# Optimization experiments

Measured on AMD Instinct MI355X. Metric: run time of the kernel, lower is better.

The kernel has to match this reference:

```python
import jax, jax.numpy as jnp
import numpy as np

B, S0 = 16, 511
D = 512    # encoder_output_dim
HG = 256   # graph_rnn_hidden_graph
HE = 256   # graph_rnn_hidden_edge (must equal HG: h_prev[0] = graph_state)
T = 128    # tag_representation_dim
M = 32     # graph_rnn_m
S = S0 + 1 # after head-sentinel prepend


def setup_inputs() -> dict:
    ks = iter(jax.random.split(jax.random.key(0), 40))
    def U(shape, fan):
        # torch RNN/Linear default init: U(-1/sqrt(fan), 1/sqrt(fan))
        return jax.random.uniform(next(ks), shape, jnp.float32, -1.0, 1.0) / np.sqrt(fan)
    return {
        'input': jax.random.normal(next(ks), (B, S0, D), jnp.float32),
        'sentinel': jax.random.normal(next(ks), (D,), jnp.float32),
        'g_Wih0': U((HG, D), HG), 'g_Whh0': U((HG, HG), HG), 'g_bih0': U((HG,), HG), 'g_bhh0': U((HG,), HG),
        'g_Wih1': U((HG, HG), HG), 'g_Whh1': U((HG, HG), HG), 'g_bih1': U((HG,), HG), 'g_bhh1': U((HG,), HG),
        'e_Wih0': U((HE, 1), HE), 'e_Whh0': U((HE, HE), HE), 'e_bih0': U((HE,), HE), 'e_bhh0': U((HE,), HE),
        'e_Wih1': U((HE, HE), HE), 'e_Whh1': U((HE, HE), HE), 'e_bih1': U((HE,), HE), 'e_bhh1': U((HE,), HE),
        'cls_W': U((1, HE), HE), 'cls_b': U((1,), HE),
        'head_W': U((T, HG), HG), 'head_b': U((T,), HG),
        'dep_W': U((T, HG), HG), 'dep_b': U((T,), HG),
        'mask': jnp.ones((B, S0), jnp.int32),
        'head_indices': jax.random.randint(next(ks), (B, S0), 0, S0, jnp.int32),
    }


def _rnn_layer(x, W_ih, W_hh, b_ih, b_hh):
    # Elman RNN layer (tanh), batch_first, h0 = 0. x: [B, S, Din] -> [B, S, H]
    xw = jnp.einsum('bsd,hd->bsh', x, W_ih) + b_ih + b_hh  # hoist input GEMM out of scan
    h0 = jnp.zeros((x.shape[0], W_hh.shape[0]), x.dtype)
    def step(h, xw_t):
        h = jnp.tanh(xw_t + h @ W_hh.T)
        return h, h
    _, ys = jax.lax.scan(step, h0, jnp.swapaxes(xw, 0, 1))
    return jnp.swapaxes(ys, 0, 1)


def _forward(input, sentinel, g_Wih0, g_Whh0, g_bih0, g_bhh0, g_Wih1, g_Whh1, g_bih1, g_bhh1,
             e_Wih0, e_Whh0, e_bih0, e_bhh0, e_Wih1, e_Whh1, e_bih1, e_bhh1,
             cls_W, cls_b, head_W, head_b, dep_W, dep_b, mask, head_indices):
    Bv = input.shape[0]
    # prepend head sentinel / prepend_ones
    x = jnp.concatenate([jnp.broadcast_to(sentinel, (Bv, 1, D)), input], axis=1)   # [B,S,D]
    mask_f = jnp.concatenate([jnp.ones((Bv, 1), mask.dtype), mask], axis=1)        # [B,S]
    # graph_pass: 2-layer tanh RNN; pad_packed_sequence zeroes padded timesteps
    h = _rnn_layer(x, g_Wih0, g_Whh0, g_bih0, g_bhh0)
    gs = _rnn_layer(h, g_Wih1, g_Whh1, g_bih1, g_bhh1)                             # [B,S,HG]
    gs = gs * mask_f[..., None].astype(gs.dtype)
    N = Bv * S
    gt = gs.reshape(N, HG)
    def estep(carry, _):
        xe, h0, h1 = carry
        h0 = jnp.tanh(xe @ e_Wih0.T + e_bih0 + e_bhh0 + h0 @ e_Whh0.T)
        h1 = jnp.tanh(h0 @ e_Wih1.T + e_bih1 + e_bhh1 + h1 @ e_Whh1.T)
        p = jax.nn.sigmoid(h1 @ cls_W.T + cls_b)   # [N,1]
        return (p, h0, h1), p[:, 0]
    init = (jnp.ones((N, 1), gs.dtype), gt, jnp.zeros((N, HE), gs.dtype))
    _, probs = jax.lax.scan(estep, init, None, length=M)                           # [M,N]
    A = jnp.concatenate([jnp.ones((1, N), gs.dtype), probs], axis=0).T.reshape(Bv, S, M + 1)
    # reshape_adj: scatter the M-band back into a [B,S,S] matrix, then transpose
    Ab = A[:, :, 1:]                                                               # [B,S,M]
    i = jnp.arange(S)[:, None]
    j = jnp.arange(S)[None, :]
    start = jnp.maximum(0, i - M)
    valid = (j >= start) & (j < i)
    midx = jnp.clip(j - start, 0, M - 1)                                           # [S,S]
    gathered = Ab[:, jnp.arange(S)[:, None], midx]                                 # [B,S,S]
    arc_logits = jnp.swapaxes(jnp.where(valid[None], gathered, jnp.zeros((), gs.dtype)), 1, 2)
    # tag heads (dropout = identity at inference)
    head_tag = jax.nn.elu(jnp.einsum('bsh,th->bst', gs, head_W) + head_b)
    dep_tag = jax.nn.elu(jnp.einsum('bsh,th->bst', gs, dep_W) + dep_b)
    return head_tag, dep_tag, arc_logits


def reference(input, sentinel, g_Wih0, g_Whh0, g_bih0, g_bhh0, g_Wih1, g_Whh1, g_bih1, g_bhh1,
              e_Wih0, e_Whh0, e_bih0, e_bhh0, e_Wih1, e_Whh1, e_bih1, e_bhh1,
              cls_W, cls_b, head_W, head_b, dep_W, dep_b, mask, head_indices):
    return _forward(input, sentinel, g_Wih0, g_Whh0, g_bih0, g_bhh0, g_Wih1, g_Whh1, g_bih1, g_bhh1,
                    e_Wih0, e_Whh0, e_bih0, e_bhh0, e_Wih1, e_Whh1, e_bih1, e_bhh1,
                    cls_W, cls_b, head_W, head_b, dep_W, dep_b, mask, head_indices)
```

## Files before the change

kernel.cpp:

```cpp
#include <hip/hip_runtime.h>

typedef unsigned short u16;
typedef short s8v __attribute__((ext_vector_type(8)));
typedef float f4v __attribute__((ext_vector_type(4)));

__device__ __forceinline__ float bf2f(u16 s) {
  unsigned u = ((unsigned)s) << 16;
  return __builtin_bit_cast(float, u);
}
__device__ __forceinline__ u16 f2bf(float f) {
  unsigned u = __builtin_bit_cast(unsigned, f);
  unsigned r = u + 0x7fffu + ((u >> 16) & 1u);
  return (u16)(r >> 16);
}
__device__ __forceinline__ s8v load8bf(const u16* p) {
  return __builtin_bit_cast(s8v, *(const uint4*)p);
}
__device__ __forceinline__ f4v mfma16(s8v a, s8v b, f4v c) {
  return __builtin_amdgcn_mfma_f32_16x16x32_bf16(a, b, c, 0, 0, 0);
}
__device__ __forceinline__ s8v pin8(s8v x) {
  union { s8v v; unsigned u[4]; } t;
  t.v = x;
  asm volatile("" : "+v"(t.u[0]), "+v"(t.u[1]), "+v"(t.u[2]), "+v"(t.u[3]));
  return t.v;
}
__device__ __forceinline__ void barrier_lds() {
  asm volatile("s_waitcnt lgkmcnt(0)\n\ts_barrier" ::: "memory");
}
__device__ __forceinline__ void cvt8(const float* p, s8v& hi, s8v& lo) {
  float4 x0 = ((const float4*)p)[0];
  float4 x1 = ((const float4*)p)[1];
  float v[8] = {x0.x, x0.y, x0.z, x0.w, x1.x, x1.y, x1.z, x1.w};
  union { s8v v; u16 a[8]; } H, L;
#pragma unroll
  for (int i = 0; i < 8; ++i) {
    u16 h = f2bf(v[i]);
    H.a[i] = h;
    L.a[i] = f2bf(v[i] - bf2f(h));
  }
  hi = H.v;
  lo = L.v;
}
__device__ __forceinline__ float fast_tanh(float x) {
  float t = __builtin_amdgcn_exp2f(x * 2.885390081777927f);
  return 1.f - 2.f * __builtin_amdgcn_rcpf(t + 1.f);
}
__device__ __forceinline__ float fast_sigmoid(float x) {
  float t = __builtin_amdgcn_exp2f(x * -1.4426950408889634f);
  return __builtin_amdgcn_rcpf(1.f + t);
}

__global__ void k_prep(const float* __restrict__ W0, const float* __restrict__ W1,
                       u16* __restrict__ whh0b, u16* __restrict__ whh1b,
                       const float* __restrict__ E0, const float* __restrict__ E1,
                       const float* __restrict__ E2, u16* __restrict__ B0,
                       u16* __restrict__ B1, u16* __restrict__ B2,
                       const float* __restrict__ gW0, u16* __restrict__ gw0hi,
                       u16* __restrict__ gw0lo, const float* __restrict__ gW1,
                       u16* __restrict__ gw1hi, u16* __restrict__ gw1lo,
                       const float* __restrict__ hW, u16* __restrict__ hWhi,
                       u16* __restrict__ hWlo, const float* __restrict__ dW,
                       u16* __restrict__ dWhi, u16* __restrict__ dWlo,
                       const int* __restrict__ mask, float* __restrict__ maskfb) {
  int t = blockIdx.x * 256 + threadIdx.x;
  if (t < 131072) {
    int layer = t >> 16;
    int idx = t & 65535;
    const float* W = layer ? W1 : W0;
    u16* dst = layer ? whh1b : whh0b;
    dst[idx] = f2bf(W[idx]);
  } else if (t < 327680) {
    int c = t - 131072;
    int which = c >> 16;
    int idx = c & 65535;
    const float* src = which == 0 ? E0 : (which == 1 ? E1 : E2);
    u16* dst = which == 0 ? B0 : (which == 1 ? B1 : B2);
    dst[idx] = f2bf(src[idx]);
  } else if (t < 589824) {
    const float* src;
    u16 *dhi, *dlo;
    int idx;
    if (t < 458752) { idx = t - 327680; src = gW0; dhi = gw0hi; dlo = gw0lo; }
    else if (t < 524288) { idx = t - 458752; src = gW1; dhi = gw1hi; dlo = gw1lo; }
    else if (t < 557056) { idx = t - 524288; src = hW; dhi = hWhi; dlo = hWlo; }
    else { idx = t - 557056; src = dW; dhi = dWhi; dlo = dWlo; }
    float v = src[idx];
    u16 h = f2bf(v);
    dhi[idx] = h;
    dlo[idx] = f2bf(v - bf2f(h));
  } else if (t < 598016) {
    int c = t - 589824;
    int s = c >> 4, b = c & 15;
    maskfb[c] = (s == 0) ? 1.f : (float)mask[b * 511 + s - 1];
  }
}

__launch_bounds__(256)
__global__ void k_xw0(const float* __restrict__ input, const float* __restrict__ sentinel,
                      const u16* __restrict__ Whi, const u16* __restrict__ Wlo,
                      const float* __restrict__ b1, const float* __restrict__ b2,
                      float* __restrict__ outxw) {
  const int l = threadIdx.x & 63;
  const int wv = threadIdx.x >> 6;
  const int l15 = l & 15, q = l >> 4;
  const int row0 = blockIdx.x * 64 + wv * 16;
  const int col0 = blockIdx.y * 64;
  int row = row0 + l15;
  int s = row & 511, b = row >> 9;
  const float* aptr = (s == 0) ? sentinel : input + (((size_t)(b * 511 + s - 1)) << 9);
  f4v acc[4];
#pragma unroll
  for (int i = 0; i < 4; ++i) acc[i] = (f4v){0.f, 0.f, 0.f, 0.f};
#pragma unroll
  for (int kt = 0; kt < 16; ++kt) {
    int k0 = kt * 32 + q * 8;
    s8v ah, al;
    cvt8(aptr + k0, ah, al);
#pragma unroll
    for (int nt = 0; nt < 4; ++nt) {
      int j = col0 + nt * 16 + l15;
      s8v wh = load8bf(Whi + ((size_t)j << 9) + k0);
      s8v wl = load8bf(Wlo + ((size_t)j << 9) + k0);
      acc[nt] = mfma16(ah, wh, acc[nt]);
      acc[nt] = mfma16(al, wh, acc[nt]);
      acc[nt] = mfma16(ah, wl, acc[nt]);
    }
  }
#pragma unroll
  for (int nt = 0; nt < 4; ++nt) {
    int col = col0 + nt * 16 + l15;
    float bias = b1[col] + b2[col];
#pragma unroll
    for (int r = 0; r < 4; ++r) {
      int rr = row0 + q * 4 + r;
      outxw[((size_t)rr << 8) + col] = acc[nt][r] + bias;
    }
  }
}

__launch_bounds__(256)
__global__ void k_gemm(const float* __restrict__ A, const u16* __restrict__ Whi,
                       const u16* __restrict__ Wlo, const float* __restrict__ b1,
                       const float* __restrict__ b2, float* __restrict__ outf,
                       int K, int J, int act) {
  const int l = threadIdx.x & 63;
  const int wv = threadIdx.x >> 6;
  const int l15 = l & 15, q = l >> 4;
  const int row0 = blockIdx.x * 64 + wv * 16;
  const int col0 = blockIdx.y * 64;
  const float* aptr = A + (size_t)(row0 + l15) * K;
  f4v acc[4];
#pragma unroll
  for (int i = 0; i < 4; ++i) acc[i] = (f4v){0.f, 0.f, 0.f, 0.f};
  const int nkt = K >> 5;
  for (int kt = 0; kt < nkt; ++kt) {
    int k0 = kt * 32 + q * 8;
    s8v ah, al;
    cvt8(aptr + k0, ah, al);
#pragma unroll
    for (int nt = 0; nt < 4; ++nt) {
      int j = col0 + nt * 16 + l15;
      s8v wh = load8bf(Whi + (size_t)j * K + k0);
      s8v wl = load8bf(Wlo + (size_t)j * K + k0);
      acc[nt] = mfma16(ah, wh, acc[nt]);
      acc[nt] = mfma16(al, wh, acc[nt]);
      acc[nt] = mfma16(ah, wl, acc[nt]);
    }
  }
#pragma unroll
  for (int nt = 0; nt < 4; ++nt) {
    int col = col0 + nt * 16 + l15;
    float bias = b1[col] + (b2 ? b2[col] : 0.f);
#pragma unroll
    for (int r = 0; r < 4; ++r) {
      int rr = row0 + q * 4 + r;
      float v = acc[nt][r] + bias;
      if (act) v = v > 0.f ? v : (__builtin_amdgcn_exp2f(v * 1.4426950408889634f) - 1.f);
      outf[(size_t)rr * J + col] = v;
    }
  }
}

__launch_bounds__(512, 2)
__global__ void k_scan_f(const float* __restrict__ xw, const u16* __restrict__ W0b,
                         const u16* __restrict__ Wxb, const u16* __restrict__ W1b,
                         const float* __restrict__ bih1, const float* __restrict__ bhh1,
                         float* __restrict__ outf, const float* __restrict__ maskf) {
  __shared__ u16 H1[2][272];
  __shared__ u16 H2[2][272];
  __shared__ float XW2[2][272];
  __shared__ float mtab[512];
  const int tid = threadIdx.x;
  const int l = tid & 63, wv = tid >> 6;
  const int l15 = l & 15, q = l >> 4;
  const int b = blockIdx.x;

  s8v w0[2][8], wx[2][8], w1[2][8];
#pragma unroll
  for (int nt = 0; nt < 2; ++nt) {
    int j = wv * 32 + nt * 16 + l15;
#pragma unroll
    for (int kt = 0; kt < 8; ++kt) {
      int off = (j << 8) + kt * 32 + q * 8;
      w0[nt][kt] = pin8(load8bf(W0b + off));
      wx[nt][kt] = pin8(load8bf(Wxb + off));
      w1[nt][kt] = pin8(load8bf(W1b + off));
    }
  }
  if (tid < 256) {
    H1[0][tid] = 0; H1[1][tid] = 0;
    H2[0][tid] = 0; H2[1][tid] = 0;
    XW2[0][tid] = 0.f; XW2[1][tid] = 0.f;
  }
  if (tid < 512) mtab[tid] = maskf[tid * 16 + b];

  const int j0 = wv * 32 + l15;
  float b2v[2];
#pragma unroll
  for (int nt = 0; nt < 2; ++nt) b2v[nt] = bih1[j0 + nt * 16] + bhh1[j0 + nt * 16];
  __syncthreads();

  const size_t nbase = (size_t)b << 9;
  const float* xrow = xw + (nbase << 8);
  const int q0 = (q == 0);

  float xA[2], xB[2];
#pragma unroll
  for (int nt = 0; nt < 2; ++nt) {
    xA[nt] = xrow[j0 + nt * 16];
    xB[nt] = xrow[256 + j0 + nt * 16];
  }

  auto STEP = [&](int g, int par, float* xc) {
    const u16* H1r = &H1[par][0];
    const u16* H2r = &H2[par][0];
    f4v a1[2], ax[2], a2[2];
#pragma unroll
    for (int nt = 0; nt < 2; ++nt) {
      a1[nt] = (f4v){xc[nt], 0.f, 0.f, 0.f};
      ax[nt] = (f4v){b2v[nt], 0.f, 0.f, 0.f};
      a2[nt] = (f4v){XW2[par][j0 + nt * 16], 0.f, 0.f, 0.f};
    }
#pragma unroll
    for (int kt = 0; kt < 8; ++kt) {
      s8v h1b = load8bf(H1r + kt * 32 + q * 8);
#pragma unroll
      for (int nt = 0; nt < 2; ++nt) {
        a1[nt] = mfma16(h1b, w0[nt][kt], a1[nt]);
        ax[nt] = mfma16(h1b, wx[nt][kt], ax[nt]);
      }
    }
#pragma unroll
    for (int kt = 0; kt < 8; ++kt) {
      s8v h2b = load8bf(H2r + kt * 32 + q * 8);
#pragma unroll
      for (int nt = 0; nt < 2; ++nt) a2[nt] = mfma16(h2b, w1[nt][kt], a2[nt]);
    }
    if (g < 512) {
      u16* Hw = &H1[1 - par][0];
#pragma unroll
      for (int nt = 0; nt < 2; ++nt) {
        float h = fast_tanh(a1[nt][0]);
        if (q0) Hw[j0 + nt * 16] = f2bf(h);
      }
    }
    if (g >= 1 && g < 513) {
      float* Xw = &XW2[1 - par][0];
#pragma unroll
      for (int nt = 0; nt < 2; ++nt)
        if (q0) Xw[j0 + nt * 16] = ax[nt][0];
    }
    if (g >= 2) {
      int t = g - 2;
      float mf = mtab[t];
      u16* Hw = &H2[1 - par][0];
      float* orow = outf + ((nbase + t) << 8);
#pragma unroll
      for (int nt = 0; nt < 2; ++nt) {
        float h = fast_tanh(a2[nt][0]);
        if (q0) {
          Hw[j0 + nt * 16] = f2bf(h);
          orow[j0 + nt * 16] = h * mf;
        }
      }
    }
  };

  for (int g = 0; g < 514; g += 2) {
    STEP(g, 0, xA);
    int sp = g + 2; if (sp > 511) sp = 511;
#pragma unroll
    for (int nt = 0; nt < 2; ++nt) xA[nt] = xrow[(sp << 8) + j0 + nt * 16];
    barrier_lds();
    STEP(g + 1, 1, xB);
    int sq = g + 3; if (sq > 511) sq = 511;
#pragma unroll
    for (int nt = 0; nt < 2; ++nt) xB[nt] = xrow[(sq << 8) + j0 + nt * 16];
    barrier_lds();
  }
}

__launch_bounds__(512, 2)
__global__ void k_enc(const float* __restrict__ gs,
                      const u16* __restrict__ W0b, const u16* __restrict__ W1b,
                      const u16* __restrict__ W2b, const float* __restrict__ wih0,
                      const float* __restrict__ bih0, const float* __restrict__ bhh0,
                      const float* __restrict__ bih1, const float* __restrict__ bhh1,
                      const float* __restrict__ clsW, const float* __restrict__ clsb,
                      float* __restrict__ Ab) {
  __shared__ __align__(16) u16 hA0[32 * 264];
  __shared__ __align__(16) u16 hA1[32 * 264];
  __shared__ float xe[32];
  __shared__ float b0v[256], w0v[256], b1v[256], clsv[256];
  __shared__ float clsbs;
  const int tid = threadIdx.x;
  const int n0 = blockIdx.x * 32;

  for (int c = tid; c < 8192; c += 512) {
    int row = c >> 8, col = c & 255;
    hA0[row * 264 + col] = f2bf(gs[(((size_t)(n0 + row)) << 8) + col]);
    hA1[row * 264 + col] = 0;
  }
  if (tid < 256) {
    b0v[tid] = bih0[tid] + bhh0[tid];
    w0v[tid] = wih0[tid];
    b1v[tid] = bih1[tid] + bhh1[tid];
    clsv[tid] = clsW[tid];
  }
  if (tid < 32) xe[tid] = 1.0f;
  if (tid == 0) clsbs = clsb[0];

  const int l = tid & 63, wv = tid >> 6;
  const int l15 = l & 15, q = l >> 4;
  const int colbase = wv * 32;

  s8v w0[2][8], w1[2][8], w2[2][8];
#pragma unroll
  for (int nt = 0; nt < 2; ++nt) {
    int jj = colbase + nt * 16 + l15;
#pragma unroll
    for (int kt = 0; kt < 8; ++kt) {
      int off = (jj << 8) + kt * 32 + q * 8;
      w0[nt][kt] = load8bf(W0b + off);
      w1[nt][kt] = load8bf(W1b + off);
      w2[nt][kt] = load8bf(W2b + off);
    }
  }
  __syncthreads();

  for (int m = 0; m < 32; ++m) {
    f4v acc[2][2];
#pragma unroll
    for (int mt = 0; mt < 2; ++mt)
#pragma unroll
      for (int nt = 0; nt < 2; ++nt) acc[mt][nt] = (f4v){0.f, 0.f, 0.f, 0.f};
#pragma unroll
    for (int kt = 0; kt < 8; ++kt) {
#pragma unroll
      for (int mt = 0; mt < 2; ++mt) {
        s8v a = __builtin_bit_cast(s8v, *(const uint4*)&hA0[(mt * 16 + l15) * 264 + kt * 32 + q * 8]);
        acc[mt][0] = mfma16(a, w0[0][kt], acc[mt][0]);
        acc[mt][1] = mfma16(a, w0[1][kt], acc[mt][1]);
      }
    }
    __syncthreads();
#pragma unroll
    for (int nt = 0; nt < 2; ++nt) {
      int col = colbase + nt * 16 + l15;
      float wc = w0v[col], bc = b0v[col];
#pragma unroll
      for (int mt = 0; mt < 2; ++mt)
#pragma unroll
        for (int r = 0; r < 4; ++r) {
          int row = mt * 16 + q * 4 + r;
          float v = acc[mt][nt][r] + xe[row] * wc + bc;
          hA0[row * 264 + col] = f2bf(fast_tanh(v));
        }
    }
    __syncthreads();
#pragma unroll
    for (int mt = 0; mt < 2; ++mt)
#pragma unroll
      for (int nt = 0; nt < 2; ++nt) acc[mt][nt] = (f4v){0.f, 0.f, 0.f, 0.f};
#pragma unroll
    for (int kt = 0; kt < 8; ++kt) {
#pragma unroll
      for (int mt = 0; mt < 2; ++mt) {
        s8v a0 = __builtin_bit_cast(s8v, *(const uint4*)&hA0[(mt * 16 + l15) * 264 + kt * 32 + q * 8]);
        s8v a1 = __builtin_bit_cast(s8v, *(const uint4*)&hA1[(mt * 16 + l15) * 264 + kt * 32 + q * 8]);
        acc[mt][0] = mfma16(a0, w1[0][kt], acc[mt][0]);
        acc[mt][1] = mfma16(a0, w1[1][kt], acc[mt][1]);
        acc[mt][0] = mfma16(a1, w2[0][kt], acc[mt][0]);
        acc[mt][1] = mfma16(a1, w2[1][kt], acc[mt][1]);
      }
    }
    __syncthreads();
#pragma unroll
    for (int nt = 0; nt < 2; ++nt) {
      int col = colbase + nt * 16 + l15;
      float bc = b1v[col];
#pragma unroll
      for (int mt = 0; mt < 2; ++mt)
#pragma unroll
        for (int r = 0; r < 4; ++r) {
          int row = mt * 16 + q * 4 + r;
          float v = acc[mt][nt][r] + bc;
          hA1[row * 264 + col] = f2bf(fast_tanh(v));
        }
    }
    __syncthreads();
    if (tid < 256) {
      int row = tid >> 3, seg = tid & 7;
      float sum = 0.f;
#pragma unroll
      for (int u = 0; u < 4; ++u) {
        int col = seg * 32 + u * 8;
#pragma unroll
        for (int e = 0; e < 8; ++e) sum += bf2f(hA1[row * 264 + col + e]) * clsv[col + e];
      }
      sum += __shfl_down(sum, 4, 8);
      sum += __shfl_down(sum, 2, 8);
      sum += __shfl_down(sum, 1, 8);
      if (seg == 0) {
        float pp = fast_sigmoid(sum + clsbs);
        xe[row] = pp;
        Ab[(((size_t)(n0 + row)) << 5) + m] = pp;
      }
    }
    __syncthreads();
  }
}

__global__ void k_arc(const float* __restrict__ Ab, float* __restrict__ out2) {
  int t = blockIdx.x * 256 + threadIdx.x;
  int b = t >> 18;
  int rem = t & 262143;
  int j = rem >> 9, i = rem & 511;
  int start = i - 32;
  if (start < 0) start = 0;
  float v = 0.f;
  if (j >= start && j < i) v = Ab[((((size_t)b << 9) + i) << 5) + (j - start)];
  out2[t] = v;
}

extern "C" void kernel_launch(void* const* d_in, const int* in_sizes, int n_in,
                              void* d_out, int out_size, void* d_ws, size_t ws_size,
                              hipStream_t stream) {
  const float* input    = (const float*)d_in[0];
  const float* sentinel = (const float*)d_in[1];
  const float* g_Wih0   = (const float*)d_in[2];
  const float* g_Whh0   = (const float*)d_in[3];
  const float* g_bih0   = (const float*)d_in[4];
  const float* g_bhh0   = (const float*)d_in[5];
  const float* g_Wih1   = (const float*)d_in[6];
  const float* g_Whh1   = (const float*)d_in[7];
  const float* g_bih1   = (const float*)d_in[8];
  const float* g_bhh1   = (const float*)d_in[9];
  const float* e_Wih0   = (const float*)d_in[10];
  const float* e_Whh0   = (const float*)d_in[11];
  const float* e_bih0   = (const float*)d_in[12];
  const float* e_bhh0   = (const float*)d_in[13];
  const float* e_Wih1   = (const float*)d_in[14];
  const float* e_Whh1   = (const float*)d_in[15];
  const float* e_bih1   = (const float*)d_in[16];
  const float* e_bhh1   = (const float*)d_in[17];
  const float* cls_W    = (const float*)d_in[18];
  const float* cls_b    = (const float*)d_in[19];
  const float* head_W   = (const float*)d_in[20];
  const float* head_b   = (const float*)d_in[21];
  const float* dep_W    = (const float*)d_in[22];
  const float* dep_b    = (const float*)d_in[23];
  const int* mask       = (const int*)d_in[24];

  float* out = (float*)d_out;
  char* ws = (char*)d_ws;
  float* xw_buf = (float*)ws;
  float* gsb    = (float*)(ws + (16u << 20));
  float* Ab     = (float*)(ws + (24u << 20));
  size_t o = (25u << 20);
  u16* whh0b   = (u16*)(ws + o); o += 128u << 10;
  u16* whh1b   = (u16*)(ws + o); o += 128u << 10;
  float* maskfb= (float*)(ws + o); o += 32u << 10;
  u16* eb0     = (u16*)(ws + o); o += 128u << 10;
  u16* eb1     = (u16*)(ws + o); o += 128u << 10;
  u16* eb2     = (u16*)(ws + o); o += 128u << 10;
  u16* gw0hi   = (u16*)(ws + o); o += 256u << 10;
  u16* gw0lo   = (u16*)(ws + o); o += 256u << 10;
  u16* gw1hi   = (u16*)(ws + o); o += 128u << 10;
  u16* gw1lo   = (u16*)(ws + o); o += 128u << 10;
  u16* hWhi    = (u16*)(ws + o); o += 64u << 10;
  u16* hWlo    = (u16*)(ws + o); o += 64u << 10;
  u16* dWhi    = (u16*)(ws + o); o += 64u << 10;
  u16* dWlo    = (u16*)(ws + o); o += 64u << 10;

  k_prep<<<2336, 256, 0, stream>>>(g_Whh0, g_Whh1, whh0b, whh1b, e_Whh0, e_Wih1, e_Whh1,
                                   eb0, eb1, eb2, g_Wih0, gw0hi, gw0lo, g_Wih1, gw1hi,
                                   gw1lo, head_W, hWhi, hWlo, dep_W, dWhi, dWlo,
                                   mask, maskfb);
  k_xw0<<<dim3(128, 4), 256, 0, stream>>>(input, sentinel, gw0hi, gw0lo, g_bih0, g_bhh0,
                                          xw_buf);
  k_scan_f<<<16, 512, 0, stream>>>(xw_buf, whh0b, gw1hi, whh1b, g_bih1, g_bhh1,
                                   gsb, maskfb);
  k_gemm<<<dim3(128, 2), 256, 0, stream>>>(gsb, hWhi, hWlo, head_b, nullptr, out,
                                           256, 128, 1);
  k_gemm<<<dim3(128, 2), 256, 0, stream>>>(gsb, dWhi, dWlo, dep_b, nullptr, out + 1048576,
                                           256, 128, 1);
  k_enc<<<256, 512, 0, stream>>>(gsb, eb0, eb1, eb2, e_Wih0, e_bih0, e_bhh0,
                                 e_bih1, e_bhh1, cls_W, cls_b, Ab);
  k_arc<<<16384, 256, 0, stream>>>(Ab, out + 2097152);
}
```

Measured before the change: 852.3 us.

## Split layer-2 scan accumulator chain and merge head/dep tag GEMM launches

```diff
diff --git a/kernel.cpp b/kernel.cpp
--- a/kernel.cpp
+++ b/kernel.cpp
@@ -140,10 +140,16 @@
 }
 
 __launch_bounds__(256)
-__global__ void k_gemm(const float* __restrict__ A, const u16* __restrict__ Whi,
-                       const u16* __restrict__ Wlo, const float* __restrict__ b1,
-                       const float* __restrict__ b2, float* __restrict__ outf,
-                       int K, int J, int act) {
+__global__ void k_gemm2(const float* __restrict__ A,
+                        const u16* __restrict__ WhiA, const u16* __restrict__ WloA,
+                        const float* __restrict__ bA, float* __restrict__ outA,
+                        const u16* __restrict__ WhiB, const u16* __restrict__ WloB,
+                        const float* __restrict__ bB, float* __restrict__ outB,
+                        int K, int J) {
+  const u16* Whi = blockIdx.z ? WhiB : WhiA;
+  const u16* Wlo = blockIdx.z ? WloB : WloA;
+  const float* b1 = blockIdx.z ? bB : bA;
+  float* outf = blockIdx.z ? outB : outA;
   const int l = threadIdx.x & 63;
   const int wv = threadIdx.x >> 6;
   const int l15 = l & 15, q = l >> 4;
@@ -171,12 +177,12 @@
 #pragma unroll
   for (int nt = 0; nt < 4; ++nt) {
     int col = col0 + nt * 16 + l15;
-    float bias = b1[col] + (b2 ? b2[col] : 0.f);
+    float bias = b1[col];
 #pragma unroll
     for (int r = 0; r < 4; ++r) {
       int rr = row0 + q * 4 + r;
       float v = acc[nt][r] + bias;
-      if (act) v = v > 0.f ? v : (__builtin_amdgcn_exp2f(v * 1.4426950408889634f) - 1.f);
+      v = v > 0.f ? v : (__builtin_amdgcn_exp2f(v * 1.4426950408889634f) - 1.f);
       outf[(size_t)rr * J + col] = v;
     }
   }
@@ -235,12 +241,13 @@
   auto STEP = [&](int g, int par, float* xc) {
     const u16* H1r = &H1[par][0];
     const u16* H2r = &H2[par][0];
-    f4v a1[2], ax[2], a2[2];
+    f4v a1[2], ax[2], a2[2], a2b[2];
 #pragma unroll
     for (int nt = 0; nt < 2; ++nt) {
       a1[nt] = (f4v){xc[nt], 0.f, 0.f, 0.f};
       ax[nt] = (f4v){b2v[nt], 0.f, 0.f, 0.f};
       a2[nt] = (f4v){XW2[par][j0 + nt * 16], 0.f, 0.f, 0.f};
+      a2b[nt] = (f4v){0.f, 0.f, 0.f, 0.f};
     }
 #pragma unroll
     for (int kt = 0; kt < 8; ++kt) {
@@ -251,12 +258,6 @@
         ax[nt] = mfma16(h1b, wx[nt][kt], ax[nt]);
       }
     }
-#pragma unroll
-    for (int kt = 0; kt < 8; ++kt) {
-      s8v h2b = load8bf(H2r + kt * 32 + q * 8);
-#pragma unroll
-      for (int nt = 0; nt < 2; ++nt) a2[nt] = mfma16(h2b, w1[nt][kt], a2[nt]);
-    }
     if (g < 512) {
       u16* Hw = &H1[1 - par][0];
 #pragma unroll
@@ -270,6 +271,15 @@
 #pragma unroll
       for (int nt = 0; nt < 2; ++nt)
         if (q0) Xw[j0 + nt * 16] = ax[nt][0];
+    }
+#pragma unroll
+    for (int kt = 0; kt < 8; ++kt) {
+      s8v h2b = load8bf(H2r + kt * 32 + q * 8);
+#pragma unroll
+      for (int nt = 0; nt < 2; ++nt) {
+        if (kt & 1) a2b[nt] = mfma16(h2b, w1[nt][kt], a2b[nt]);
+        else        a2[nt]  = mfma16(h2b, w1[nt][kt], a2[nt]);
+      }
     }
     if (g >= 2) {
       int t = g - 2;
@@ -278,7 +288,7 @@
       float* orow = outf + ((nbase + t) << 8);
 #pragma unroll
       for (int nt = 0; nt < 2; ++nt) {
-        float h = fast_tanh(a2[nt][0]);
+        float h = fast_tanh(a2[nt][0] + a2b[nt][0]);
         if (q0) {
           Hw[j0 + nt * 16] = f2bf(h);
           orow[j0 + nt * 16] = h * mf;
@@ -502,10 +512,9 @@
                                           xw_buf);
   k_scan_f<<<16, 512, 0, stream>>>(xw_buf, whh0b, gw1hi, whh1b, g_bih1, g_bhh1,
                                    gsb, maskfb);
-  k_gemm<<<dim3(128, 2), 256, 0, stream>>>(gsb, hWhi, hWlo, head_b, nullptr, out,
-                                           256, 128, 1);
-  k_gemm<<<dim3(128, 2), 256, 0, stream>>>(gsb, dWhi, dWlo, dep_b, nullptr, out + 1048576,
-                                           256, 128, 1);
+  k_gemm2<<<dim3(128, 2, 2), 256, 0, stream>>>(gsb, hWhi, hWlo, head_b, out,
+                                               dWhi, dWlo, dep_b, out + 1048576,
+                                               256, 128);
   k_enc<<<256, 512, 0, stream>>>(gsb, eb0, eb1, eb2, e_Wih0, e_bih0, e_bhh0,
                                  e_bih1, e_bhh1, cls_W, cls_b, Ab);
   k_arc<<<16384, 256, 0, stream>>>(Ab, out + 2097152);
```

New measurement: 867.7 us. No clear change (+1.8%).
